# Optimization experiments

Measured on AMD Instinct MI355X. Metric: run time of the kernel, lower is better.

The kernel has to match this reference:

```python
import jax, jax.numpy as jnp
import numpy as np

B, S, D, BS = 256, 256, 448, 32
NB = D // BS  # 14 diagonal blocks


def setup_inputs() -> dict:
    key = jax.random.key(0)
    ks = jax.random.split(key, 9)
    xavier = float(np.sqrt(6.0 / (D + D)))
    inp = {
        "x": jax.random.normal(ks[0], (B, S, D), jnp.float32),
        "W_q": jax.random.uniform(ks[1], (D, D), jnp.float32, -xavier, xavier),
        "W_k": jax.random.uniform(ks[2], (D, D), jnp.float32, -xavier, xavier),
        "W_v": jax.random.uniform(ks[3], (D, D), jnp.float32, -xavier, xavier),
        "W_o": jax.random.uniform(ks[4], (D, D), jnp.float32, -xavier, xavier),
        "SSM_A": jnp.tril(jax.random.normal(ks[5], (D, D), jnp.float32) * 0.001),
        "SSM_B": jnp.tril(jax.random.normal(ks[6], (D, D), jnp.float32) * 0.001),
        "SSM_C": jnp.tril(jax.random.normal(ks[7], (D, D), jnp.float32) * 0.001),
        "dynamic_weight": jnp.full((1,), 0.5, jnp.float32),  # torch init value
        "ln_gamma": jnp.ones((D,), jnp.float32),
        "ln_beta": jnp.zeros((D,), jnp.float32),
    }
    return inp


def _diag_blocks(M):
    # extract the NB diagonal 32x32 blocks: [NB, BS, BS]
    idx = jnp.arange(NB)
    return M.reshape(NB, BS, NB, BS)[idx, :, idx, :]


def _block_linear(x, M):
    # block-diagonal matmul, vectorized over all 14 blocks at once
    xr = x.reshape(B, S, NB, BS)
    return jnp.einsum('bsni,nij->bsnj', xr, _diag_blocks(M)).reshape(B, S, D)


def _block_quadratic(x, M):
    # einsum('bsi,ij,bsk->bsj') per block == (x_blk @ M_blk) * sum_k(x_blk) * 0.1
    xr = x.reshape(B, S, NB, BS)
    y = jnp.einsum('bsni,nij->bsnj', xr, _diag_blocks(M))
    y = y * (jnp.sum(xr, axis=-1, keepdims=True) * 0.1)
    return y.reshape(B, S, D)


def _layer_norm(x, gamma, beta):
    mu = jnp.mean(x, axis=-1, keepdims=True)
    var = jnp.mean(jnp.square(x - mu), axis=-1, keepdims=True)
    return (x - mu) * jax.lax.rsqrt(var + 1e-5) * gamma + beta


def reference(x, W_q, W_k, W_v, W_o, SSM_A, SSM_B, SSM_C, dynamic_weight, ln_gamma, ln_beta):
    q = jnp.einsum('bsi,id->bsd', x, W_q)
    k = jnp.einsum('bsi,id->bsd', x, W_k)
    v = jnp.einsum('bsi,id->bsd', x, W_v)
    dw = jax.nn.sigmoid(dynamic_weight)  # sigmoid(0.5)=0.622 -> blended branch (seq_len == threshold)
    ssm_lin = _layer_norm(
        _block_linear(q, SSM_A) + _block_linear(k, SSM_B) + _block_linear(v, SSM_C),
        ln_gamma, ln_beta)
    ssm_quad = _layer_norm(
        _block_quadratic(q, SSM_A) + _block_quadratic(k, SSM_B) + _block_quadratic(v, SSM_C),
        ln_gamma, ln_beta)
    ssm = dw * ssm_quad + (1.0 - dw) * ssm_lin
    ssm = ssm + x  # residual; dropout is identity in eval mode
    return jnp.einsum('bsd,do->bso', ssm, W_o)
```

## Files before the change

### kernel.cpp

```cpp
#include <hip/hip_runtime.h>
#include <hip/hip_bf16.h>


typedef unsigned short u16;
typedef unsigned int u32;
typedef __bf16 bf16x8 __attribute__((ext_vector_type(8)));
typedef float f32x4 __attribute__((ext_vector_type(4)));

#define D_DIM 448
#define M_DIM 65536
#define NCAT 1386
#define NCAT_PAD 1408
#define N2_PAD 512

#define CVT_BLKS 28672
#define WO_BLKS 896
#define WCAT_BLKS 1408

__device__ __forceinline__ u16 f2bf(float f) {
    union { float f; u32 u; } v; v.f = f;
    u32 u = v.u;
    u32 r = (u + 0x7fffu + ((u >> 16) & 1u)) >> 16;
    return (u16)r;
}
__device__ __forceinline__ float bf2f(u16 h) {
    union { u32 u; float f; } v; v.u = ((u32)h) << 16;
    return v.f;
}

__device__ __forceinline__ void load_lds16(const void* g, void* l) {
    __builtin_amdgcn_global_load_lds(
        (const __attribute__((address_space(1))) void*)g,
        (__attribute__((address_space(3))) void*)l, 16, 0, 0);
}

__global__ __launch_bounds__(256) void prep_all(
    const float* __restrict__ x,
    const float* __restrict__ Wq, const float* __restrict__ Wk, const float* __restrict__ Wv,
    const float* __restrict__ Wo,
    const float* __restrict__ SA, const float* __restrict__ SB, const float* __restrict__ SC,
    u16* __restrict__ Xbf, u16* __restrict__ WcatT, u16* __restrict__ WoT)
{
    const int bid = blockIdx.x;
    const int tid = threadIdx.x;

    if (bid < CVT_BLKS) {
        const size_t i = ((size_t)bid * 256 + tid) * 4;
        float4 v = *reinterpret_cast<const float4*>(x + i);
        u32 lo = (u32)f2bf(v.x) | ((u32)f2bf(v.y) << 16);
        u32 hi = (u32)f2bf(v.z) | ((u32)f2bf(v.w) << 16);
        u32* p = reinterpret_cast<u32*>(Xbf + i);
        p[0] = lo; p[1] = hi;
        return;
    }
    if (bid < CVT_BLKS + WO_BLKS) {
        const int idx = (bid - CVT_BLKS) * 256 + tid;
        const int o = idx / D_DIM, d = idx % D_DIM;
        WoT[idx] = (o < D_DIM) ? f2bf(Wo[(size_t)d * D_DIM + o]) : (u16)0;
        return;
    }
    const int j = bid - (CVT_BLKS + WO_BLKS);
    u16* dst = WcatT + (size_t)j * D_DIM;
    if (j >= NCAT) {
        for (int t = tid; t < D_DIM; t += 256) dst[t] = 0;
        return;
    }
    if (j < 3 * D_DIM) {
        const int g = j / D_DIM, jj = j % D_DIM, n = jj >> 5;
        const float* W = (g == 0) ? Wq : (g == 1) ? Wk : Wv;
        const float* Mm = (g == 0) ? SA : (g == 1) ? SB : SC;
        __shared__ float av[32];
        if (tid < 32) av[tid] = Mm[(size_t)(n * 32 + tid) * D_DIM + jj];
        __syncthreads();
        for (int t = tid; t < D_DIM; t += 256) {
            const float* wrow = W + (size_t)t * D_DIM + n * 32;
            float s = 0.f;
            #pragma unroll
            for (int l = 0; l < 32; ++l) s += wrow[l] * av[l];
            dst[t] = f2bf(s);
        }
    } else {
        const int js = j - 3 * D_DIM;
        const int g = js / 14, n = js % 14;
        const float* W = (g == 0) ? Wq : (g == 1) ? Wk : Wv;
        for (int t = tid; t < D_DIM; t += 256) {
            const float* wrow = W + (size_t)t * D_DIM + n * 32;
            float s = 0.f;
            #pragma unroll
            for (int l = 0; l < 32; ++l) s += wrow[l];
            dst[t] = f2bf(0.1f * s);
        }
    }
}

template<bool BF16OUT>
__global__ __launch_bounds__(256) void gemm_bt(
    const u16* __restrict__ A,
    const u16* __restrict__ Bt,
    void* __restrict__ Cout,
    int ldc, int nreal, int ncolblk)
{
    __shared__ u16 lA0[4096], lB0[4096], lA1[4096], lB1[4096];
    const int tid = threadIdx.x;
    const int wave = tid >> 6, lane = tid & 63;

    const int cpx = gridDim.x >> 3;
    const int bid = blockIdx.x;
    const int t = (bid & 7) * cpx + (bid >> 3);
    const int bx = t % ncolblk, by = t / ncolblk;
    const int brow = by * 128, bcol = bx * 128;
    const int wr = wave >> 1, wc = wave & 1;

    f32x4 acc[4][4];
    #pragma unroll
    for (int i = 0; i < 4; ++i)
        #pragma unroll
        for (int jj = 0; jj < 4; ++jj) {
            f32x4 z = {0.f, 0.f, 0.f, 0.f};
            acc[i][jj] = z;
        }

    const int lrow = lane & 15;
    const int kgrp = (lane >> 4) << 3;

    const int c0 = wave * 128 + lane;
    const int c1 = c0 + 64;
    const int row0 = c0 >> 2, kk0 = (c0 & 3) << 3;
    const int row1 = c1 >> 2, kk1 = (c1 & 3) << 3;
    const u16* ga0 = A  + (size_t)(brow + row0) * D_DIM + kk0;
    const u16* ga1 = A  + (size_t)(brow + row1) * D_DIM + kk1;
    const u16* gb0 = Bt + (size_t)(bcol + row0) * D_DIM + kk0;
    const u16* gb1 = Bt + (size_t)(bcol + row1) * D_DIM + kk1;
    const int d0 = wave * 1024, d1 = wave * 1024 + 512;

#define STAGE(LA, LB, koff) do { \
    load_lds16(ga0 + (koff), &LA[d0]); \
    load_lds16(ga1 + (koff), &LA[d1]); \
    load_lds16(gb0 + (koff), &LB[d0]); \
    load_lds16(gb1 + (koff), &LB[d1]); \
} while (0)

#define COMPUTE(LA, LB) do { \
    bf16x8 af[4]; \
    _Pragma("unroll") \
    for (int mi = 0; mi < 4; ++mi) \
        af[mi] = *reinterpret_cast<const bf16x8*>(&LA[(wr * 64 + mi * 16 + lrow) * 32 + kgrp]); \
    _Pragma("unroll") \
    for (int ni = 0; ni < 4; ++ni) { \
        bf16x8 bfr = *reinterpret_cast<const bf16x8*>(&LB[(wc * 64 + ni * 16 + lrow) * 32 + kgrp]); \
        _Pragma("unroll") \
        for (int mi = 0; mi < 4; ++mi) \
            acc[mi][ni] = __builtin_amdgcn_mfma_f32_16x16x32_bf16(af[mi], bfr, acc[mi][ni], 0, 0, 0); \
    } \
} while (0)

    STAGE(lA0, lB0, 0);
    __syncthreads();

    for (int kt = 0; kt < 14; kt += 2) {
        STAGE(lA1, lB1, (kt + 1) * 32);
        COMPUTE(lA0, lB0);
        __syncthreads();
        if (kt + 2 < 14) STAGE(lA0, lB0, (kt + 2) * 32);
        COMPUTE(lA1, lB1);
        __syncthreads();
    }
#undef STAGE
#undef COMPUTE

    const int rbase = brow + wr * 64 + ((lane >> 4) << 2);
    const int cbase = bcol + wc * 64 + (lane & 15);
    #pragma unroll
    for (int mi = 0; mi < 4; ++mi) {
        #pragma unroll
        for (int ni = 0; ni < 4; ++ni) {
            const int col = cbase + ni * 16;
            #pragma unroll
            for (int r = 0; r < 4; ++r) {
                const int row = rbase + mi * 16 + r;
                const float v = acc[mi][ni][r];
                if (BF16OUT) {
                    ((u16*)Cout)[(size_t)row * ldc + col] = f2bf(v);
                } else {
                    if (col < nreal)
                        ((float*)Cout)[(size_t)row * nreal + col] = v;
                }
            }
        }
    }
}

__global__ __launch_bounds__(256) void ssm_epilogue(
    const u16* __restrict__ Z, const u16* __restrict__ xb,
    const float* __restrict__ gamma, const float* __restrict__ beta,
    const float* __restrict__ dynw, u16* __restrict__ ssm)
{
    const int row = blockIdx.x * 4 + (threadIdx.x >> 6);
    const int lane = threadIdx.x & 63;
    const u16* zr = Z + (size_t)row * NCAT_PAD;
    const float dwv = 1.0f / (1.0f + __expf(-dynw[0]));
    const bool act = lane < 56;
    const int j0 = lane * 8;
    const int n = lane >> 2;

    float sv = (lane < 42) ? bf2f(zr[1344 + lane]) : 0.f;
    const float sA = __shfl(sv, n);
    const float sB = __shfl(sv, 14 + n);
    const float sC = __shfl(sv, 28 + n);

    float L[8], Q[8];
    float s0 = 0.f, s1 = 0.f, s2 = 0.f, s3 = 0.f;
    if (act) {
        uint4 va = *reinterpret_cast<const uint4*>(zr + j0);
        uint4 vb = *reinterpret_cast<const uint4*>(zr + 448 + j0);
        uint4 vc = *reinterpret_cast<const uint4*>(zr + 896 + j0);
        const u32* pa = reinterpret_cast<const u32*>(&va);
        const u32* pb = reinterpret_cast<const u32*>(&vb);
        const u32* pc = reinterpret_cast<const u32*>(&vc);
        #pragma unroll
        for (int w = 0; w < 4; ++w) {
            #pragma unroll
            for (int h = 0; h < 2; ++h) {
                const int i = w * 2 + h;
                const float a = bf2f((u16)((pa[w] >> (16 * h)) & 0xffffu));
                const float b = bf2f((u16)((pb[w] >> (16 * h)) & 0xffffu));
                const float c = bf2f((u16)((pc[w] >> (16 * h)) & 0xffffu));
                const float Lv = a + b + c;
                const float Qv = a * sA + b * sB + c * sC;
                L[i] = Lv; Q[i] = Qv;
                s0 += Lv; s1 += Lv * Lv; s2 += Qv; s3 += Qv * Qv;
            }
        }
    } else {
        #pragma unroll
        for (int i = 0; i < 8; ++i) { L[i] = 0.f; Q[i] = 0.f; }
    }
    #pragma unroll
    for (int off = 32; off > 0; off >>= 1) {
        s0 += __shfl_xor(s0, off);
        s1 += __shfl_xor(s1, off);
        s2 += __shfl_xor(s2, off);
        s3 += __shfl_xor(s3, off);
    }
    const float inv = 1.0f / 448.0f;
    const float mu0 = s0 * inv, mu1 = s2 * inv;
    const float rs0 = rsqrtf(fmaxf(s1 * inv - mu0 * mu0, 0.f) + 1e-5f);
    const float rs1 = rsqrtf(fmaxf(s3 * inv - mu1 * mu1, 0.f) + 1e-5f);

    if (act) {
        float4 g0 = *reinterpret_cast<const float4*>(gamma + j0);
        float4 g1 = *reinterpret_cast<const float4*>(gamma + j0 + 4);
        float4 b0 = *reinterpret_cast<const float4*>(beta + j0);
        float4 b1 = *reinterpret_cast<const float4*>(beta + j0 + 4);
        float gv[8] = {g0.x, g0.y, g0.z, g0.w, g1.x, g1.y, g1.z, g1.w};
        float bv[8] = {b0.x, b0.y, b0.z, b0.w, b1.x, b1.y, b1.z, b1.w};
        uint4 vx = *reinterpret_cast<const uint4*>(xb + (size_t)row * D_DIM + j0);
        const u32* px = reinterpret_cast<const u32*>(&vx);
        u32 outw[4];
        #pragma unroll
        for (int w = 0; w < 4; ++w) {
            u16 h0, h1;
            {
                const int i = w * 2;
                const float xr = bf2f((u16)(px[w] & 0xffffu));
                const float ln = (L[i] - mu0) * rs0 * gv[i] + bv[i];
                const float qn = (Q[i] - mu1) * rs1 * gv[i] + bv[i];
                h0 = f2bf(dwv * qn + (1.0f - dwv) * ln + xr);
            }
            {
                const int i = w * 2 + 1;
                const float xr = bf2f((u16)(px[w] >> 16));
                const float ln = (L[i] - mu0) * rs0 * gv[i] + bv[i];
                const float qn = (Q[i] - mu1) * rs1 * gv[i] + bv[i];
                h1 = f2bf(dwv * qn + (1.0f - dwv) * ln + xr);
            }
            outw[w] = (u32)h0 | ((u32)h1 << 16);
        }
        uint4 ov = {outw[0], outw[1], outw[2], outw[3]};
        *reinterpret_cast<uint4*>(ssm + (size_t)row * D_DIM + j0) = ov;
    }
}

extern "C" void kernel_launch(void* const* d_in, const int* in_sizes, int n_in,
                              void* d_out, int out_size, void* d_ws, size_t ws_size,
                              hipStream_t stream) {
    const float* x    = (const float*)d_in[0];
    const float* Wq   = (const float*)d_in[1];
    const float* Wk   = (const float*)d_in[2];
    const float* Wv   = (const float*)d_in[3];
    const float* Wo   = (const float*)d_in[4];
    const float* SA   = (const float*)d_in[5];
    const float* SB   = (const float*)d_in[6];
    const float* SC   = (const float*)d_in[7];
    const float* dynw = (const float*)d_in[8];
    const float* gma  = (const float*)d_in[9];
    const float* bta  = (const float*)d_in[10];
    float* out = (float*)d_out;

    char* ws = (char*)d_ws;
    u16* Xbf   = (u16*)(ws);
    u16* WcatT = (u16*)(ws + 58720256);
    u16* WoT   = (u16*)(ws + 59981824);
    u16* Z     = (u16*)(ws + 60440576);

    prep_all<<<dim3(CVT_BLKS + WO_BLKS + WCAT_BLKS), dim3(256), 0, stream>>>(
        x, Wq, Wk, Wv, Wo, SA, SB, SC, Xbf, WcatT, WoT);

    gemm_bt<true><<<dim3(5632), dim3(256), 0, stream>>>(
        Xbf, WcatT, (void*)Z, NCAT_PAD, NCAT_PAD, 11);

    ssm_epilogue<<<dim3(M_DIM / 4), dim3(256), 0, stream>>>(Z, Xbf, gma, bta, dynw, Xbf);

    gemm_bt<false><<<dim3(2048), dim3(256), 0, stream>>>(
        Xbf, WoT, (void*)out, 448, 448, 4);
}
```

Baseline: 432.4 us.

## Replace 128x128 GEMM with 8-wave 256x256 swizzled-LDS phased pipeline

Both bf16 GEMMs now use a new kernel with 512 threads and 256x256 output tiles. It uses a K step of 64, double-buffered 128KB dynamic LDS with an XOR swizzle, and a four-phase schedule. That schedule interleaves half-tile loads with MFMA bursts and raises wave priority during the MFMAs. The intermediate Z buffer stride drops to 1392 and the concatenated weight is padded to 1536 rows, so it tiles evenly by 256. The aim is more operand reuse per LDS byte, fewer bank conflicts and better overlap of memory with compute. The cost is large LDS use, which limits occupancy to one block per CU, and tile-quantization waste on the padded columns.

Result: no change. 429.8 us (-0.6%).

```diff
diff --git a/kernel.cpp b/kernel.cpp
--- a/kernel.cpp
+++ b/kernel.cpp
@@ -10,24 +10,23 @@
 #define D_DIM 448
 #define M_DIM 65536
 #define NCAT 1386
-#define NCAT_PAD 1408
+#define NWCAT 1536
+#define ZSTRIDE 1392
 #define N2_PAD 512
 
 #define CVT_BLKS 28672
 #define WO_BLKS 896
-#define WCAT_BLKS 1408
+#define WCAT_BLKS 1536
 
 __device__ __forceinline__ u16 f2bf(float f) {
     union { float f; u32 u; } v; v.f = f;
     u32 u = v.u;
-    u32 r = (u + 0x7fffu + ((u >> 16) & 1u)) >> 16;
-    return (u16)r;
+    return (u16)((u + 0x7fffu + ((u >> 16) & 1u)) >> 16);
 }
 __device__ __forceinline__ float bf2f(u16 h) {
     union { u32 u; float f; } v; v.u = ((u32)h) << 16;
     return v.f;
 }
-
 __device__ __forceinline__ void load_lds16(const void* g, void* l) {
     __builtin_amdgcn_global_load_lds(
         (const __attribute__((address_space(1))) void*)g,
@@ -93,101 +92,154 @@
     }
 }
 
+
+#define VMW(N) do { asm volatile("s_waitcnt vmcnt(" #N ")" ::: "memory"); } while (0)
+
 template<bool BF16OUT>
-__global__ __launch_bounds__(256) void gemm_bt(
+__global__ __launch_bounds__(512, 2) void gemm8p(
     const u16* __restrict__ A,
     const u16* __restrict__ Bt,
     void* __restrict__ Cout,
-    int ldc, int nreal, int ncolblk)
+    int ldc, int ncstore, int ncolblk)
 {
-    __shared__ u16 lA0[4096], lB0[4096], lA1[4096], lB1[4096];
+    extern __shared__ char ldsc[];
     const int tid = threadIdx.x;
     const int wave = tid >> 6, lane = tid & 63;
+    const int lrow = lane & 15;
+    const int wr = wave >> 2, wc = wave & 3;
 
     const int cpx = gridDim.x >> 3;
     const int bid = blockIdx.x;
-    const int t = (bid & 7) * cpx + (bid >> 3);
-    const int bx = t % ncolblk, by = t / ncolblk;
-    const int brow = by * 128, bcol = bx * 128;
-    const int wr = wave >> 1, wc = wave & 1;
-
-    f32x4 acc[4][4];
-    #pragma unroll
-    for (int i = 0; i < 4; ++i)
-        #pragma unroll
-        for (int jj = 0; jj < 4; ++jj) {
-            f32x4 z = {0.f, 0.f, 0.f, 0.f};
-            acc[i][jj] = z;
-        }
-
-    const int lrow = lane & 15;
-    const int kgrp = (lane >> 4) << 3;
-
-    const int c0 = wave * 128 + lane;
-    const int c1 = c0 + 64;
-    const int row0 = c0 >> 2, kk0 = (c0 & 3) << 3;
-    const int row1 = c1 >> 2, kk1 = (c1 & 3) << 3;
-    const u16* ga0 = A  + (size_t)(brow + row0) * D_DIM + kk0;
-    const u16* ga1 = A  + (size_t)(brow + row1) * D_DIM + kk1;
-    const u16* gb0 = Bt + (size_t)(bcol + row0) * D_DIM + kk0;
-    const u16* gb1 = Bt + (size_t)(bcol + row1) * D_DIM + kk1;
-    const int d0 = wave * 1024, d1 = wave * 1024 + 512;
-
-#define STAGE(LA, LB, koff) do { \
-    load_lds16(ga0 + (koff), &LA[d0]); \
-    load_lds16(ga1 + (koff), &LA[d1]); \
-    load_lds16(gb0 + (koff), &LB[d0]); \
-    load_lds16(gb1 + (koff), &LB[d1]); \
+    const int tt = (bid & 7) * cpx + (bid >> 3);
+    const int bx = tt % ncolblk, by = tt / ncolblk;
+    const int brow = by * 256, bcol = bx * 256;
+
+    const int c0 = wave * 64 + lane;
+    const int r0 = c0 >> 3, r1 = r0 + 64;
+    const int sc0 = ((((c0 & 7) << 4) ^ ((r0 & 7) << 4)) >> 1);
+    const int sc1 = ((((c0 & 7) << 4) ^ ((r1 & 7) << 4)) >> 1);
+    const int off0 = r0 * D_DIM + sc0;
+    const int off1 = r1 * D_DIM + sc1;
+
+    u32 aoff[4][2], boff[2][2];
+    #pragma unroll
+    for (int mi = 0; mi < 4; ++mi) {
+        const int r = wr * 64 + mi * 16 + lrow;
+        #pragma unroll
+        for (int ks = 0; ks < 2; ++ks) {
+            const int cb = ks * 64 + ((lane >> 4) << 4);
+            aoff[mi][ks] = (u32)(((r << 7) + cb) ^ ((r & 7) << 4));
+        }
+    }
+    #pragma unroll
+    for (int ni = 0; ni < 2; ++ni) {
+        const int r = wc * 32 + ni * 16 + lrow;
+        #pragma unroll
+        for (int ks = 0; ks < 2; ++ks) {
+            const int cb = ks * 64 + ((lane >> 4) << 4);
+            boff[ni][ks] = (u32)(((r << 7) + cb) ^ ((r & 7) << 4));
+        }
+    }
+
+    f32x4 acc[2][4][2][2];
+    #pragma unroll
+    for (int a0 = 0; a0 < 2; ++a0)
+        #pragma unroll
+        for (int a1 = 0; a1 < 4; ++a1)
+            #pragma unroll
+            for (int a2 = 0; a2 < 2; ++a2)
+                #pragma unroll
+                for (int a3 = 0; a3 < 2; ++a3) {
+                    f32x4 z = {0.f, 0.f, 0.f, 0.f};
+                    acc[a0][a1][a2][a3] = z;
+                }
+
+#define STAGE_HALF(PTR, G0, ISB, H, K0, NBUF) do { \
+    const u16* _gs = (PTR) + (size_t)((G0) + (H) * 128) * D_DIM + (K0); \
+    char* _lb = ldsc + (NBUF) * 65536 + (ISB) * 32768 + (H) * 16384 + wave * 1024; \
+    load_lds16(_gs + off0, _lb); \
+    load_lds16(_gs + off1, _lb + 8192); \
 } while (0)
 
-#define COMPUTE(LA, LB) do { \
-    bf16x8 af[4]; \
-    _Pragma("unroll") \
-    for (int mi = 0; mi < 4; ++mi) \
-        af[mi] = *reinterpret_cast<const bf16x8*>(&LA[(wr * 64 + mi * 16 + lrow) * 32 + kgrp]); \
-    _Pragma("unroll") \
-    for (int ni = 0; ni < 4; ++ni) { \
-        bf16x8 bfr = *reinterpret_cast<const bf16x8*>(&LB[(wc * 64 + ni * 16 + lrow) * 32 + kgrp]); \
+#define PHASE(BUF, MH, NH, VMEND, ...) do { \
+    bf16x8 af[4][2], bfr[2][2]; \
+    { \
+        const char* _ab = ldsc + (BUF) * 65536 + (MH) * 16384; \
         _Pragma("unroll") \
         for (int mi = 0; mi < 4; ++mi) \
-            acc[mi][ni] = __builtin_amdgcn_mfma_f32_16x16x32_bf16(af[mi], bfr, acc[mi][ni], 0, 0, 0); \
+            _Pragma("unroll") \
+            for (int ks = 0; ks < 2; ++ks) \
+                af[mi][ks] = *reinterpret_cast<const bf16x8*>(_ab + aoff[mi][ks]); \
+        const char* _bb = ldsc + (BUF) * 65536 + 32768 + (NH) * 16384; \
+        _Pragma("unroll") \
+        for (int ni = 0; ni < 2; ++ni) \
+            _Pragma("unroll") \
+            for (int ks = 0; ks < 2; ++ks) \
+                bfr[ni][ks] = *reinterpret_cast<const bf16x8*>(_bb + boff[ni][ks]); \
     } \
+    __VA_ARGS__; \
+    __builtin_amdgcn_s_barrier(); \
+    asm volatile("s_waitcnt lgkmcnt(0)" ::: "memory"); \
+    __builtin_amdgcn_sched_barrier(0); \
+    __builtin_amdgcn_s_setprio(1); \
+    _Pragma("unroll") \
+    for (int ni = 0; ni < 2; ++ni) \
+        _Pragma("unroll") \
+        for (int mi = 0; mi < 4; ++mi) \
+            _Pragma("unroll") \
+            for (int ks = 0; ks < 2; ++ks) \
+                acc[MH][mi][NH][ni] = __builtin_amdgcn_mfma_f32_16x16x32_bf16( \
+                    af[mi][ks], bfr[ni][ks], acc[MH][mi][NH][ni], 0, 0, 0); \
+    __builtin_amdgcn_s_setprio(0); \
+    VMEND; \
+    __builtin_amdgcn_s_barrier(); \
 } while (0)
 
-    STAGE(lA0, lB0, 0);
-    __syncthreads();
-
-    for (int kt = 0; kt < 14; kt += 2) {
-        STAGE(lA1, lB1, (kt + 1) * 32);
-        COMPUTE(lA0, lB0);
-        __syncthreads();
-        if (kt + 2 < 14) STAGE(lA0, lB0, (kt + 2) * 32);
-        COMPUTE(lA1, lB1);
-        __syncthreads();
-    }
-#undef STAGE
-#undef COMPUTE
-
-    const int rbase = brow + wr * 64 + ((lane >> 4) << 2);
-    const int cbase = bcol + wc * 64 + (lane & 15);
-    #pragma unroll
-    for (int mi = 0; mi < 4; ++mi) {
-        #pragma unroll
-        for (int ni = 0; ni < 4; ++ni) {
-            const int col = cbase + ni * 16;
-            #pragma unroll
-            for (int r = 0; r < 4; ++r) {
-                const int row = rbase + mi * 16 + r;
-                const float v = acc[mi][ni][r];
-                if (BF16OUT) {
-                    ((u16*)Cout)[(size_t)row * ldc + col] = f2bf(v);
-                } else {
-                    if (col < nreal)
-                        ((float*)Cout)[(size_t)row * nreal + col] = v;
+    STAGE_HALF(A,  brow, 0, 0, 0, 0);
+    STAGE_HALF(Bt, bcol, 1, 0, 0, 0);
+    STAGE_HALF(Bt, bcol, 1, 1, 0, 0);
+    STAGE_HALF(A,  brow, 0, 1, 0, 0);
+    VMW(4);
+    __builtin_amdgcn_s_barrier();
+
+    for (int t = 0; t < 6; ++t) {
+        const int buf = t & 1, nbuf = buf ^ 1;
+        const int k1 = (t + 1) * 64;
+        PHASE(buf, 0, 0, VMW(4), STAGE_HALF(A,  brow, 0, 0, k1, nbuf));
+        PHASE(buf, 0, 1, VMW(4), STAGE_HALF(Bt, bcol, 1, 0, k1, nbuf));
+        PHASE(buf, 1, 1, (void)0, STAGE_HALF(Bt, bcol, 1, 1, k1, nbuf));
+        PHASE(buf, 1, 0, VMW(4), STAGE_HALF(A,  brow, 0, 1, k1, nbuf));
+    }
+    PHASE(0, 0, 0, VMW(2), (void)0);
+    PHASE(0, 0, 1, VMW(0), (void)0);
+    PHASE(0, 1, 1, (void)0, (void)0);
+    PHASE(0, 1, 0, (void)0, (void)0);
+
+#undef PHASE
+#undef STAGE_HALF
+
+    #pragma unroll
+    for (int mh = 0; mh < 2; ++mh)
+        #pragma unroll
+        for (int mi = 0; mi < 4; ++mi)
+            #pragma unroll
+            for (int nh = 0; nh < 2; ++nh)
+                #pragma unroll
+                for (int ni = 0; ni < 2; ++ni) {
+                    const int col = bcol + nh * 128 + wc * 32 + ni * 16 + lrow;
+                    const int rbase = brow + mh * 128 + wr * 64 + mi * 16 + ((lane >> 4) << 2);
+                    #pragma unroll
+                    for (int r = 0; r < 4; ++r) {
+                        const float v = acc[mh][mi][nh][ni][r];
+                        if (BF16OUT) {
+                            if (col < ncstore)
+                                ((u16*)Cout)[(size_t)(rbase + r) * ldc + col] = f2bf(v);
+                        } else {
+                            if (col < ncstore)
+                                ((float*)Cout)[(size_t)(rbase + r) * ldc + col] = v;
+                        }
+                    }
                 }
-            }
-        }
-    }
 }
 
 __global__ __launch_bounds__(256) void ssm_epilogue(
@@ -197,7 +249,7 @@
 {
     const int row = blockIdx.x * 4 + (threadIdx.x >> 6);
     const int lane = threadIdx.x & 63;
-    const u16* zr = Z + (size_t)row * NCAT_PAD;
+    const u16* zr = Z + (size_t)row * ZSTRIDE;
     const float dwv = 1.0f / (1.0f + __expf(-dynw[0]));
     const bool act = lane < 56;
     const int j0 = lane * 8;
@@ -300,17 +352,22 @@
     char* ws = (char*)d_ws;
     u16* Xbf   = (u16*)(ws);
     u16* WcatT = (u16*)(ws + 58720256);
-    u16* WoT   = (u16*)(ws + 59981824);
-    u16* Z     = (u16*)(ws + 60440576);
+    u16* WoT   = (u16*)(ws + 60096512);
+    u16* Z     = (u16*)(ws + 60555264);
+
+    (void)hipFuncSetAttribute(reinterpret_cast<const void*>(gemm8p<true>),
+                              hipFuncAttributeMaxDynamicSharedMemorySize, 131072);
+    (void)hipFuncSetAttribute(reinterpret_cast<const void*>(gemm8p<false>),
+                              hipFuncAttributeMaxDynamicSharedMemorySize, 131072);
 
     prep_all<<<dim3(CVT_BLKS + WO_BLKS + WCAT_BLKS), dim3(256), 0, stream>>>(
         x, Wq, Wk, Wv, Wo, SA, SB, SC, Xbf, WcatT, WoT);
 
-    gemm_bt<true><<<dim3(5632), dim3(256), 0, stream>>>(
-        Xbf, WcatT, (void*)Z, NCAT_PAD, NCAT_PAD, 11);
+    gemm8p<true><<<dim3(1536), dim3(512), 131072, stream>>>(
+        Xbf, WcatT, (void*)Z, ZSTRIDE, ZSTRIDE, 6);
 
     ssm_epilogue<<<dim3(M_DIM / 4), dim3(256), 0, stream>>>(Z, Xbf, gma, bta, dynw, Xbf);
 
-    gemm_bt<false><<<dim3(2048), dim3(256), 0, stream>>>(
-        Xbf, WoT, (void*)out, 448, 448, 4);
-}
+    gemm8p<false><<<dim3(512), dim3(512), 131072, stream>>>(
+        Xbf, WoT, (void*)out, 448, 448, 2);
+}
```
